# Kernel optimization log

Hardware: AMD Instinct MI355X
Metric: run time of the kernel (lower is better)

## Reference

```python
import jax, jax.numpy as jnp
import numpy as np

B, D, T = 16, 512, 4096
N_CB, K, CDIM = 9, 1024, 8
EPS = 1e-12  # F.normalize eps


def setup_inputs() -> dict:
    key = jax.random.key(0)
    ks = jax.random.split(key, 6)
    z = jax.random.normal(ks[0], (B, D, T), dtype=jnp.float32)
    # Effective (post weight-norm) 1x1-conv weights per codebook, stacked over N_CB
    w_in = jax.random.normal(ks[1], (N_CB, CDIM, D), dtype=jnp.float32) * 0.02
    b_in = jax.random.normal(ks[2], (N_CB, CDIM), dtype=jnp.float32) * 0.02
    w_out = jax.random.normal(ks[3], (N_CB, D, CDIM), dtype=jnp.float32) * 0.02
    b_out = jax.random.normal(ks[4], (N_CB, D), dtype=jnp.float32) * 0.02
    codebooks = jax.random.normal(ks[5], (N_CB, K, CDIM), dtype=jnp.float32)
    return {"z": z, "w_in": w_in, "b_in": b_in, "w_out": w_out,
            "b_out": b_out, "codebooks": codebooks}


def _l2norm(x):
    return x / jnp.maximum(jnp.linalg.norm(x, axis=-1, keepdims=True), EPS)


def reference(z, w_in, b_in, w_out, b_out, codebooks):
    """Eval-mode RVQ forward with all n_codebooks quantizers (mask all-True).
    Returns (z_q, codes, latents, commitment_loss, codebook_loss)."""
    Bz, _, Tz = z.shape

    def step(carry, params):
        residual, zq_acc, cl, cbl = carry
        wi, bi, wo, bo, cb = params
        # in_proj: 1x1 conv input_dim -> codebook_dim
        z_e = jnp.einsum('cd,bdt->bct', wi, residual) + bi[None, :, None]  # B,CDIM,T
        enc = z_e.transpose(0, 2, 1).reshape(-1, z_e.shape[1])            # (B*T),CDIM
        en = _l2norm(enc)
        cbn = _l2norm(cb)
        # squared euclidean distance on l2-normalized vectors (cosine dist)
        dist = ((en * en).sum(1, keepdims=True)
                - 2.0 * (en @ cbn.T)
                + (cbn * cbn).sum(1)[None, :])                            # (B*T),K
        idx = jnp.argmin(dist, axis=1).reshape(Bz, Tz)                    # B,T
        z_q_i = cb[idx].transpose(0, 2, 1)                                # B,CDIM,T (raw codebook)
        cl = cl + jnp.mean((z_e - jax.lax.stop_gradient(z_q_i)) ** 2, axis=(1, 2)).mean()
        cbl = cbl + jnp.mean((z_q_i - jax.lax.stop_gradient(z_e)) ** 2, axis=(1, 2)).mean()
        # straight-through estimator
        z_q_st = z_e + jax.lax.stop_gradient(z_q_i - z_e)
        z_q_out = jnp.einsum('dc,bct->bdt', wo, z_q_st) + bo[None, :, None]  # B,D,T
        return (residual - z_q_out, zq_acc + z_q_out, cl, cbl), (idx, z_e)

    init = (z, jnp.zeros_like(z), jnp.float32(0.0), jnp.float32(0.0))
    (_, z_q, cl, cbl), (codes, latents) = jax.lax.scan(
        step, init, (w_in, b_in, w_out, b_out, codebooks))
    codes = codes.transpose(1, 0, 2)                         # B,N,T
    latents = latents.transpose(1, 0, 2, 3).reshape(Bz, -1, Tz)  # B,N*CDIM,T
    return z_q, codes, latents, cl, cbl
```

## Files before the change

### kernel.cpp

```cpp
#include <hip/hip_runtime.h>
#include <math.h>

#define Bz  16
#define Dz  512
#define Tz  4096
#define NCB 9
#define Kz  1024
#define CD  8

static const unsigned long long OZQ   = 0ull;
static const unsigned long long OCODE = 33554432ull;
static const unsigned long long OLAT  = 34144256ull;
static const unsigned long long OCL   = 38862848ull;

#define WS_CBN2_OFF (NCB * CD * Kz)

__global__ __launch_bounds__(1024) void rvq_prep(const float* __restrict__ cb,
                                                 float* __restrict__ ws,
                                                 float* __restrict__ out) {
    const int i = blockIdx.x;
    const int k = threadIdx.x;
    const float* row = cb + ((size_t)i * Kz + k) * CD;
    float v[CD];
#pragma unroll
    for (int c = 0; c < CD; ++c) v[c] = row[c];
    float ss = 0.f;
#pragma unroll
    for (int c = 0; c < CD; ++c) ss += v[c] * v[c];
    const float den = fmaxf(sqrtf(ss), 1e-12f);
    float cb2 = 0.f;
#pragma unroll
    for (int c = 0; c < CD; ++c) {
        float e = v[c] / den;
        ws[((size_t)i * CD + c) * Kz + k] = e;
        cb2 += e * e;
    }
    ws[WS_CBN2_OFF + (size_t)i * Kz + k] = cb2;
    if (i == 0 && k == 0) { out[OCL] = 0.f; out[OCL + 1] = 0.f; }
}

__global__
__attribute__((amdgpu_flat_work_group_size(512, 512), amdgpu_waves_per_eu(4, 4)))
void rvq_main(
    const float* __restrict__ z,
    const float* __restrict__ w_in,
    const float* __restrict__ b_in,
    const float* __restrict__ w_out,
    const float* __restrict__ b_out,
    const float* __restrict__ cb,
    const float* __restrict__ ws,
    float* __restrict__ out)
{
    __shared__ float s_win[64 * 68];
    __shared__ float s_cbnT[8 * 64 * 20];
    __shared__ float s_cbn2[Kz];
    __shared__ float s_tr[32 * 68];
    __shared__ float s_lat[8 * 33];
    __shared__ float s_code[NCB * 32];
    __shared__ float s_red[8];

    const int tid  = threadIdx.x;
    const int wave = tid >> 6;
    const int lane = tid & 63;
    const int bb   = blockIdx.x;
    const int b    = bb >> 7;
    const int t0blk = (bb & 127) << 5;
    const int mycol = lane & 3;

    const size_t zbase = (size_t)b * Dz * Tz + t0blk;

    float res4[4][8];
#pragma unroll 1
    for (int c = 0; c < 8; ++c) {
        {
            const int r = tid >> 3;
            const int u = (tid & 7) * 4;
            float4 v = *(const float4*)(z + zbase + (size_t)(c * 64 + r) * Tz + u);
            s_tr[(u + 0) * 68 + r] = v.x;
            s_tr[(u + 1) * 68 + r] = v.y;
            s_tr[(u + 2) * 68 + r] = v.z;
            s_tr[(u + 3) * 68 + r] = v.w;
        }
        __syncthreads();
        if ((lane >> 3) == c) {
            const int lr = (lane & 7) * 8;
#pragma unroll
            for (int col = 0; col < 4; ++col)
#pragma unroll
                for (int j = 0; j < 8; ++j)
                    res4[col][j] = s_tr[(wave * 4 + col) * 68 + lr + j];
        }
        __syncthreads();
    }

    float lsum = 0.f;

#pragma unroll 1
    for (int i = 0; i < NCB; ++i) {
        __syncthreads();
        if (i > 0 && tid < 256) {
            const int c2 = tid >> 5, u = tid & 31;
            out[OLAT + ((size_t)b * 72 + (i - 1) * 8 + c2) * Tz + t0blk + u] =
                s_lat[c2 * 33 + u];
        }
        {
            const float4* src = (const float4*)(w_in + (size_t)i * 4096);
#pragma unroll
            for (int it = 0; it < 2; ++it) {
                int e4 = tid + it * 512;
                float4 v = src[e4];
                int e = e4 * 4, c = e >> 9, d = e & 511;
                *(float4*)&s_win[(d >> 3) * 68 + c * 8 + (d & 7)] = v;
            }
            const float4* srcT = (const float4*)(ws + (size_t)i * 8192);
#pragma unroll
            for (int it = 0; it < 4; ++it) {
                int e4 = tid + it * 512;
                float4 v = srcT[e4];
                int e = e4 * 4, c = e >> 10, k = e & 1023;
                *(float4*)&s_cbnT[c * 1280 + (k >> 4) * 20 + (k & 15)] = v;
            }
            if (tid < 256) {
                const float4* s2 = (const float4*)(ws + WS_CBN2_OFF + (size_t)i * Kz);
                ((float4*)s_cbn2)[tid] = s2[tid];
            }
        }
        __syncthreads();

        float z_own[8];
#pragma unroll
        for (int c = 0; c < 8; ++c) {
            const float* wl = &s_win[lane * 68 + c * 8];
            float4 a = *(const float4*)wl;
            float4 b4 = *(const float4*)(wl + 4);
            float w8[8] = {a.x, a.y, a.z, a.w, b4.x, b4.y, b4.z, b4.w};
            float q[4];
#pragma unroll
            for (int col = 0; col < 4; ++col) {
                float s = 0.f;
#pragma unroll
                for (int j = 0; j < 8; ++j) s = fmaf(w8[j], res4[col][j], s);
                q[col] = s;
            }
#pragma unroll
            for (int col = 0; col < 4; ++col) {
                q[col] += __shfl_xor(q[col], 1, 64);
                q[col] += __shfl_xor(q[col], 2, 64);
            }
            float v = q[0];
            v = (mycol == 1) ? q[1] : v;
            v = (mycol == 2) ? q[2] : v;
            v = (mycol == 3) ? q[3] : v;
#pragma unroll
            for (int off = 4; off <= 32; off <<= 1) v += __shfl_xor(v, off, 64);
            z_own[c] = v + b_in[i * 8 + c];
        }

        {
            int cc = lane >> 2;
            float v = z_own[0];
#pragma unroll
            for (int c = 1; c < 8; ++c) v = (cc == c) ? z_own[c] : v;
            if (lane < 32) s_lat[cc * 33 + wave * 4 + mycol] = v;
        }

        float ss = 0.f;
#pragma unroll
        for (int c = 0; c < 8; ++c) ss += z_own[c] * z_own[c];
        const float den = fmaxf(sqrtf(ss), 1e-12f);
        float en_own[8];
#pragma unroll
        for (int c = 0; c < 8; ++c) en_own[c] = z_own[c] / den;

        float en4[4][8];
        const int qbase = lane & ~3;
#pragma unroll
        for (int g = 0; g < 4; ++g) {
#pragma unroll
            for (int c = 0; c < 8; ++c) en4[g][c] = __shfl(en_own[c], qbase + g, 64);
        }

        float best[4]; int bidx[4];
#pragma unroll
        for (int g = 0; g < 4; ++g) { best[g] = 1e30f; bidx[g] = 0; }
#pragma unroll
        for (int mq = 0; mq < 4; ++mq) {
            float4 c2 = *(const float4*)&s_cbn2[lane * 16 + mq * 4];
            float dots[4][4];
#pragma unroll
            for (int g = 0; g < 4; ++g)
#pragma unroll
                for (int q = 0; q < 4; ++q) dots[g][q] = 0.f;
#pragma unroll
            for (int c = 0; c < 8; ++c) {
                float4 v = *(const float4*)&s_cbnT[c * 1280 + lane * 20 + mq * 4];
#pragma unroll
                for (int g = 0; g < 4; ++g) {
                    dots[g][0] = fmaf(en4[g][c], v.x, dots[g][0]);
                    dots[g][1] = fmaf(en4[g][c], v.y, dots[g][1]);
                    dots[g][2] = fmaf(en4[g][c], v.z, dots[g][2]);
                    dots[g][3] = fmaf(en4[g][c], v.w, dots[g][3]);
                }
            }
#pragma unroll
            for (int q = 0; q < 4; ++q) {
                const int kk = lane * 16 + mq * 4 + q;
                const float cb2q = (q == 0) ? c2.x : (q == 1) ? c2.y : (q == 2) ? c2.z : c2.w;
#pragma unroll
                for (int g = 0; g < 4; ++g) {
                    float dist = fmaf(-2.f, dots[g][q], cb2q);
                    if (dist < best[g]) { best[g] = dist; bidx[g] = kk; }
                }
            }
        }
#pragma unroll
        for (int off = 1; off <= 32; off <<= 1) {
#pragma unroll
            for (int g = 0; g < 4; ++g) {
                float ob = __shfl_xor(best[g], off, 64);
                int   oi = __shfl_xor(bidx[g], off, 64);
                if (ob < best[g] || (ob == best[g] && oi < bidx[g])) {
                    best[g] = ob; bidx[g] = oi;
                }
            }
        }

        float cbq[4][8];
#pragma unroll
        for (int g = 0; g < 4; ++g) {
            const float* cr = cb + ((size_t)i * Kz + bidx[g]) * CD;
            float4 a = *(const float4*)cr;
            float4 b4 = *(const float4*)(cr + 4);
            cbq[g][0] = a.x;  cbq[g][1] = a.y;  cbq[g][2] = a.z;  cbq[g][3] = a.w;
            cbq[g][4] = b4.x; cbq[g][5] = b4.y; cbq[g][6] = b4.z; cbq[g][7] = b4.w;
        }

#pragma unroll
        for (int g = 0; g < 4; ++g) {
            if (lane == g) {
#pragma unroll
                for (int c = 0; c < 8; ++c) {
                    float dd = z_own[c] - cbq[g][c];
                    lsum = fmaf(dd, dd, lsum);
                }
            }
        }

        {
            float v = (float)bidx[0];
            v = (lane == 1) ? (float)bidx[1] : v;
            v = (lane == 2) ? (float)bidx[2] : v;
            v = (lane == 3) ? (float)bidx[3] : v;
            if (lane < 4) s_code[i * 32 + wave * 4 + lane] = v;
        }

        {
            const float* wo = w_out + (size_t)i * 4096 + (size_t)lane * 64;
            const float* bo = b_out + (size_t)i * Dz + lane * 8;
            float4 bA = *(const float4*)bo;
            float4 bB = *(const float4*)(bo + 4);
            float bv[8] = {bA.x, bA.y, bA.z, bA.w, bB.x, bB.y, bB.z, bB.w};
#pragma unroll
            for (int j = 0; j < 8; ++j) {
                float4 wa = *(const float4*)(wo + j * 8);
                float4 wb = *(const float4*)(wo + j * 8 + 4);
                float wr[8] = {wa.x, wa.y, wa.z, wa.w, wb.x, wb.y, wb.z, wb.w};
#pragma unroll
                for (int g = 0; g < 4; ++g) {
                    float s = 0.f;
#pragma unroll
                    for (int c = 0; c < 8; ++c) s = fmaf(wr[c], cbq[g][c], s);
                    res4[g][j] -= (s + bv[j]);
                }
            }
        }
    }

    __syncthreads();
    if (tid < 256) {
        const int c2 = tid >> 5, u = tid & 31;
        out[OLAT + ((size_t)b * 72 + 8 * 8 + c2) * Tz + t0blk + u] = s_lat[c2 * 33 + u];
    }
    if (tid < NCB * 32) {
        const int i2 = tid >> 5, u = tid & 31;
        out[OCODE + ((size_t)b * NCB + i2) * Tz + t0blk + u] = s_code[i2 * 32 + u];
    }

#pragma unroll 1
    for (int c = 0; c < 8; ++c) {
        if ((lane >> 3) == c) {
            const int lr = (lane & 7) * 8;
#pragma unroll
            for (int col = 0; col < 4; ++col)
#pragma unroll
                for (int j = 0; j < 8; ++j)
                    s_tr[(wave * 4 + col) * 68 + lr + j] = res4[col][j];
        }
        __syncthreads();
        {
            const int r = tid >> 3;
            const int u = (tid & 7) * 4;
            float4 zv = *(const float4*)(z + zbase + (size_t)(c * 64 + r) * Tz + u);
            float4 v;
            v.x = zv.x - s_tr[(u + 0) * 68 + r];
            v.y = zv.y - s_tr[(u + 1) * 68 + r];
            v.z = zv.z - s_tr[(u + 2) * 68 + r];
            v.w = zv.w - s_tr[(u + 3) * 68 + r];
            *(float4*)(out + OZQ + zbase + (size_t)(c * 64 + r) * Tz + u) = v;
        }
        __syncthreads();
    }

#pragma unroll
    for (int off = 1; off <= 32; off <<= 1) lsum += __shfl_xor(lsum, off, 64);
    if (lane == 0) s_red[wave] = lsum;
    __syncthreads();
    if (tid == 0) {
        float t = 0.f;
#pragma unroll
        for (int w2 = 0; w2 < 8; ++w2) t += s_red[w2];
        t *= (1.f / 524288.f);
        atomicAdd(&out[OCL], t);
        atomicAdd(&out[OCL + 1], t);
    }
}

extern "C" void kernel_launch(void* const* d_in, const int* in_sizes, int n_in,
                              void* d_out, int out_size, void* d_ws, size_t ws_size,
                              hipStream_t stream) {
    (void)in_sizes; (void)n_in; (void)out_size; (void)ws_size;
    const float* z     = (const float*)d_in[0];
    const float* w_in  = (const float*)d_in[1];
    const float* b_in  = (const float*)d_in[2];
    const float* w_out = (const float*)d_in[3];
    const float* b_out = (const float*)d_in[4];
    const float* cb    = (const float*)d_in[5];
    float* ws  = (float*)d_ws;
    float* out = (float*)d_out;

    rvq_prep<<<NCB, 1024, 0, stream>>>(cb, ws, out);
    rvq_main<<<2048, 512, 0, stream>>>(z, w_in, b_in, w_out, b_out, cb, ws, out);
}
```

Baseline: 1.283 ms.

## Use 1024-thread blocks with two time columns per wave and alias transpose buffer

Doubles the threads per block from 512 to 1024 so each wave owns 2 time columns instead of 4, which halves per-thread register state (residuals, dots, best indices) and the argmin work per wave. The transpose scratch buffer is aliased onto the codebook LDS region to save shared memory, and the load and reduction loops are retiled for 16 waves. Each wave now scans the full codebook for only 2 columns, so codebook LDS reads per useful distance double. The launch-bounds change also drops the explicit waves-per-EU hint.

Result: slower. 1.370 ms (+6.8%).

```diff
diff --git a/kernel.cpp b/kernel.cpp
--- a/kernel.cpp
+++ b/kernel.cpp
@@ -39,8 +39,7 @@
     if (i == 0 && k == 0) { out[OCL] = 0.f; out[OCL + 1] = 0.f; }
 }
 
-__global__
-__attribute__((amdgpu_flat_work_group_size(512, 512), amdgpu_waves_per_eu(4, 4)))
+__global__ __launch_bounds__(1024)
 void rvq_main(
     const float* __restrict__ z,
     const float* __restrict__ w_in,
@@ -54,10 +53,11 @@
     __shared__ float s_win[64 * 68];
     __shared__ float s_cbnT[8 * 64 * 20];
     __shared__ float s_cbn2[Kz];
-    __shared__ float s_tr[32 * 68];
     __shared__ float s_lat[8 * 33];
     __shared__ float s_code[NCB * 32];
-    __shared__ float s_red[8];
+    __shared__ float s_red[16];
+
+    float* s_tr = s_cbnT;
 
     const int tid  = threadIdx.x;
     const int wave = tid >> 6;
@@ -65,30 +65,30 @@
     const int bb   = blockIdx.x;
     const int b    = bb >> 7;
     const int t0blk = (bb & 127) << 5;
-    const int mycol = lane & 3;
+    const int mycol = lane & 1;
 
     const size_t zbase = (size_t)b * Dz * Tz + t0blk;
 
-    float res4[4][8];
+    float res2[2][8];
 #pragma unroll 1
-    for (int c = 0; c < 8; ++c) {
+    for (int c = 0; c < 4; ++c) {
         {
             const int r = tid >> 3;
             const int u = (tid & 7) * 4;
-            float4 v = *(const float4*)(z + zbase + (size_t)(c * 64 + r) * Tz + u);
-            s_tr[(u + 0) * 68 + r] = v.x;
-            s_tr[(u + 1) * 68 + r] = v.y;
-            s_tr[(u + 2) * 68 + r] = v.z;
-            s_tr[(u + 3) * 68 + r] = v.w;
-        }
-        __syncthreads();
-        if ((lane >> 3) == c) {
-            const int lr = (lane & 7) * 8;
-#pragma unroll
-            for (int col = 0; col < 4; ++col)
+            float4 v = *(const float4*)(z + zbase + (size_t)(c * 128 + r) * Tz + u);
+            s_tr[(u + 0) * 132 + r] = v.x;
+            s_tr[(u + 1) * 132 + r] = v.y;
+            s_tr[(u + 2) * 132 + r] = v.z;
+            s_tr[(u + 3) * 132 + r] = v.w;
+        }
+        __syncthreads();
+        if ((lane >> 4) == c) {
+            const int lr = (lane & 15) * 8;
+#pragma unroll
+            for (int col = 0; col < 2; ++col)
 #pragma unroll
                 for (int j = 0; j < 8; ++j)
-                    res4[col][j] = s_tr[(wave * 4 + col) * 68 + lr + j];
+                    res2[col][j] = s_tr[(wave * 2 + col) * 132 + lr + j];
         }
         __syncthreads();
     }
@@ -105,17 +105,16 @@
         }
         {
             const float4* src = (const float4*)(w_in + (size_t)i * 4096);
-#pragma unroll
-            for (int it = 0; it < 2; ++it) {
-                int e4 = tid + it * 512;
+            {
+                int e4 = tid;
                 float4 v = src[e4];
                 int e = e4 * 4, c = e >> 9, d = e & 511;
                 *(float4*)&s_win[(d >> 3) * 68 + c * 8 + (d & 7)] = v;
             }
             const float4* srcT = (const float4*)(ws + (size_t)i * 8192);
 #pragma unroll
-            for (int it = 0; it < 4; ++it) {
-                int e4 = tid + it * 512;
+            for (int it = 0; it < 2; ++it) {
+                int e4 = tid + it * 1024;
                 float4 v = srcT[e4];
                 int e = e4 * 4, c = e >> 10, k = e & 1023;
                 *(float4*)&s_cbnT[c * 1280 + (k >> 4) * 20 + (k & 15)] = v;
@@ -134,34 +133,28 @@
             float4 a = *(const float4*)wl;
             float4 b4 = *(const float4*)(wl + 4);
             float w8[8] = {a.x, a.y, a.z, a.w, b4.x, b4.y, b4.z, b4.w};
-            float q[4];
-#pragma unroll
-            for (int col = 0; col < 4; ++col) {
+            float q[2];
+#pragma unroll
+            for (int col = 0; col < 2; ++col) {
                 float s = 0.f;
 #pragma unroll
-                for (int j = 0; j < 8; ++j) s = fmaf(w8[j], res4[col][j], s);
+                for (int j = 0; j < 8; ++j) s = fmaf(w8[j], res2[col][j], s);
                 q[col] = s;
             }
-#pragma unroll
-            for (int col = 0; col < 4; ++col) {
-                q[col] += __shfl_xor(q[col], 1, 64);
-                q[col] += __shfl_xor(q[col], 2, 64);
-            }
-            float v = q[0];
-            v = (mycol == 1) ? q[1] : v;
-            v = (mycol == 2) ? q[2] : v;
-            v = (mycol == 3) ? q[3] : v;
-#pragma unroll
-            for (int off = 4; off <= 32; off <<= 1) v += __shfl_xor(v, off, 64);
+            q[0] += __shfl_xor(q[0], 1, 64);
+            q[1] += __shfl_xor(q[1], 1, 64);
+            float v = mycol ? q[1] : q[0];
+#pragma unroll
+            for (int off = 2; off <= 32; off <<= 1) v += __shfl_xor(v, off, 64);
             z_own[c] = v + b_in[i * 8 + c];
         }
 
         {
-            int cc = lane >> 2;
+            int cc = lane >> 1;
             float v = z_own[0];
 #pragma unroll
             for (int c = 1; c < 8; ++c) v = (cc == c) ? z_own[c] : v;
-            if (lane < 32) s_lat[cc * 33 + wave * 4 + mycol] = v;
+            if (lane < 16) s_lat[cc * 33 + wave * 2 + mycol] = v;
         }
 
         float ss = 0.f;
@@ -172,34 +165,34 @@
 #pragma unroll
         for (int c = 0; c < 8; ++c) en_own[c] = z_own[c] / den;
 
-        float en4[4][8];
-        const int qbase = lane & ~3;
-#pragma unroll
-        for (int g = 0; g < 4; ++g) {
-#pragma unroll
-            for (int c = 0; c < 8; ++c) en4[g][c] = __shfl(en_own[c], qbase + g, 64);
-        }
-
-        float best[4]; int bidx[4];
-#pragma unroll
-        for (int g = 0; g < 4; ++g) { best[g] = 1e30f; bidx[g] = 0; }
+        float en2[2][8];
+        const int qb = lane & ~1;
+#pragma unroll
+        for (int g = 0; g < 2; ++g) {
+#pragma unroll
+            for (int c = 0; c < 8; ++c) en2[g][c] = __shfl(en_own[c], qb + g, 64);
+        }
+
+        float best[2]; int bidx[2];
+#pragma unroll
+        for (int g = 0; g < 2; ++g) { best[g] = 1e30f; bidx[g] = 0; }
 #pragma unroll
         for (int mq = 0; mq < 4; ++mq) {
             float4 c2 = *(const float4*)&s_cbn2[lane * 16 + mq * 4];
-            float dots[4][4];
-#pragma unroll
-            for (int g = 0; g < 4; ++g)
+            float dots[2][4];
+#pragma unroll
+            for (int g = 0; g < 2; ++g)
 #pragma unroll
                 for (int q = 0; q < 4; ++q) dots[g][q] = 0.f;
 #pragma unroll
             for (int c = 0; c < 8; ++c) {
                 float4 v = *(const float4*)&s_cbnT[c * 1280 + lane * 20 + mq * 4];
 #pragma unroll
-                for (int g = 0; g < 4; ++g) {
-                    dots[g][0] = fmaf(en4[g][c], v.x, dots[g][0]);
-                    dots[g][1] = fmaf(en4[g][c], v.y, dots[g][1]);
-                    dots[g][2] = fmaf(en4[g][c], v.z, dots[g][2]);
-                    dots[g][3] = fmaf(en4[g][c], v.w, dots[g][3]);
+                for (int g = 0; g < 2; ++g) {
+                    dots[g][0] = fmaf(en2[g][c], v.x, dots[g][0]);
+                    dots[g][1] = fmaf(en2[g][c], v.y, dots[g][1]);
+                    dots[g][2] = fmaf(en2[g][c], v.z, dots[g][2]);
+                    dots[g][3] = fmaf(en2[g][c], v.w, dots[g][3]);
                 }
             }
 #pragma unroll
@@ -207,7 +200,7 @@
                 const int kk = lane * 16 + mq * 4 + q;
                 const float cb2q = (q == 0) ? c2.x : (q == 1) ? c2.y : (q == 2) ? c2.z : c2.w;
 #pragma unroll
-                for (int g = 0; g < 4; ++g) {
+                for (int g = 0; g < 2; ++g) {
                     float dist = fmaf(-2.f, dots[g][q], cb2q);
                     if (dist < best[g]) { best[g] = dist; bidx[g] = kk; }
                 }
@@ -216,7 +209,7 @@
 #pragma unroll
         for (int off = 1; off <= 32; off <<= 1) {
 #pragma unroll
-            for (int g = 0; g < 4; ++g) {
+            for (int g = 0; g < 2; ++g) {
                 float ob = __shfl_xor(best[g], off, 64);
                 int   oi = __shfl_xor(bidx[g], off, 64);
                 if (ob < best[g] || (ob == best[g] && oi < bidx[g])) {
@@ -225,9 +218,9 @@
             }
         }
 
-        float cbq[4][8];
-#pragma unroll
-        for (int g = 0; g < 4; ++g) {
+        float cbq[2][8];
+#pragma unroll
+        for (int g = 0; g < 2; ++g) {
             const float* cr = cb + ((size_t)i * Kz + bidx[g]) * CD;
             float4 a = *(const float4*)cr;
             float4 b4 = *(const float4*)(cr + 4);
@@ -236,7 +229,7 @@
         }
 
 #pragma unroll
-        for (int g = 0; g < 4; ++g) {
+        for (int g = 0; g < 2; ++g) {
             if (lane == g) {
 #pragma unroll
                 for (int c = 0; c < 8; ++c) {
@@ -249,9 +242,7 @@
         {
             float v = (float)bidx[0];
             v = (lane == 1) ? (float)bidx[1] : v;
-            v = (lane == 2) ? (float)bidx[2] : v;
-            v = (lane == 3) ? (float)bidx[3] : v;
-            if (lane < 4) s_code[i * 32 + wave * 4 + lane] = v;
+            if (lane < 2) s_code[i * 32 + wave * 2 + lane] = v;
         }
 
         {
@@ -266,11 +257,11 @@
                 float4 wb = *(const float4*)(wo + j * 8 + 4);
                 float wr[8] = {wa.x, wa.y, wa.z, wa.w, wb.x, wb.y, wb.z, wb.w};
 #pragma unroll
-                for (int g = 0; g < 4; ++g) {
+                for (int g = 0; g < 2; ++g) {
                     float s = 0.f;
 #pragma unroll
                     for (int c = 0; c < 8; ++c) s = fmaf(wr[c], cbq[g][c], s);
-                    res4[g][j] -= (s + bv[j]);
+                    res2[g][j] -= (s + bv[j]);
                 }
             }
         }
@@ -287,26 +278,26 @@
     }
 
 #pragma unroll 1
-    for (int c = 0; c < 8; ++c) {
-        if ((lane >> 3) == c) {
-            const int lr = (lane & 7) * 8;
-#pragma unroll
-            for (int col = 0; col < 4; ++col)
+    for (int c = 0; c < 4; ++c) {
+        if ((lane >> 4) == c) {
+            const int lr = (lane & 15) * 8;
+#pragma unroll
+            for (int col = 0; col < 2; ++col)
 #pragma unroll
                 for (int j = 0; j < 8; ++j)
-                    s_tr[(wave * 4 + col) * 68 + lr + j] = res4[col][j];
+                    s_tr[(wave * 2 + col) * 132 + lr + j] = res2[col][j];
         }
         __syncthreads();
         {
             const int r = tid >> 3;
             const int u = (tid & 7) * 4;
-            float4 zv = *(const float4*)(z + zbase + (size_t)(c * 64 + r) * Tz + u);
+            float4 zv = *(const float4*)(z + zbase + (size_t)(c * 128 + r) * Tz + u);
             float4 v;
-            v.x = zv.x - s_tr[(u + 0) * 68 + r];
-            v.y = zv.y - s_tr[(u + 1) * 68 + r];
-            v.z = zv.z - s_tr[(u + 2) * 68 + r];
-            v.w = zv.w - s_tr[(u + 3) * 68 + r];
-            *(float4*)(out + OZQ + zbase + (size_t)(c * 64 + r) * Tz + u) = v;
+            v.x = zv.x - s_tr[(u + 0) * 132 + r];
+            v.y = zv.y - s_tr[(u + 1) * 132 + r];
+            v.z = zv.z - s_tr[(u + 2) * 132 + r];
+            v.w = zv.w - s_tr[(u + 3) * 132 + r];
+            *(float4*)(out + OZQ + zbase + (size_t)(c * 128 + r) * Tz + u) = v;
         }
         __syncthreads();
     }
@@ -318,7 +309,7 @@
     if (tid == 0) {
         float t = 0.f;
 #pragma unroll
-        for (int w2 = 0; w2 < 8; ++w2) t += s_red[w2];
+        for (int w2 = 0; w2 < 16; ++w2) t += s_red[w2];
         t *= (1.f / 524288.f);
         atomicAdd(&out[OCL], t);
         atomicAdd(&out[OCL + 1], t);
@@ -339,5 +330,5 @@
     float* out = (float*)d_out;
 
     rvq_prep<<<NCB, 1024, 0, stream>>>(cb, ws, out);
-    rvq_main<<<2048, 512, 0, stream>>>(z, w_in, b_in, w_out, b_out, cb, ws, out);
+    rvq_main<<<2048, 1024, 0, stream>>>(z, w_in, b_in, w_out, b_out, cb, ws, out);
 }
```
